# Kernel optimization log

Measured on AMD Instinct MI355X. Metric: run time of the kernel, lower is better.

The kernel has to match this reference:

```python
import jax, jax.numpy as jnp
import numpy as np

N, E, D, H, G, C = 50000, 600000, 128, 128, 512, 1000
HP = H // 5  # attention-MLP bottleneck (hidden_dim // 5)


def setup_inputs() -> dict:
    key = jax.random.key(0)
    ks = jax.random.split(key, 18)
    cfg_nodes = jax.random.normal(ks[0], (N, D), jnp.float32)
    cfg_relations = jax.random.randint(ks[1], (2, E), 0, N, dtype=jnp.int32)
    pos = jnp.sort(jax.random.randint(ks[2], (G + 1,), 0, N, dtype=jnp.int32))
    node_pos = pos.at[0].set(0).at[-1].set(N)

    def lin(k, fi, fo):
        return jax.random.normal(k, (fi, fo), jnp.float32) / np.sqrt(fi)

    return dict(
        cfg_nodes=cfg_nodes, cfg_relations=cfg_relations, node_pos=node_pos,
        # GATConv layer 1 (in=D, out=H, heads=1)
        W_g1=lin(ks[3], D, H),
        att_src1=jax.random.normal(ks[4], (H,), jnp.float32) / np.sqrt(H),
        att_dst1=jax.random.normal(ks[5], (H,), jnp.float32) / np.sqrt(H),
        b_g1=jnp.zeros((H,), jnp.float32),
        # GATConv layer 2 (in=H, out=H, heads=1, concat=False)
        W_g2=lin(ks[6], H, H),
        att_src2=jax.random.normal(ks[7], (H,), jnp.float32) / np.sqrt(H),
        att_dst2=jax.random.normal(ks[8], (H,), jnp.float32) / np.sqrt(H),
        b_g2=jnp.zeros((H,), jnp.float32),
        # GraphLocalAttention projection MLP
        Wp1=lin(ks[9], H, HP), bp1=jnp.zeros((HP,), jnp.float32),
        Wp2=jax.random.normal(ks[10], (HP,), jnp.float32) / np.sqrt(HP),
        bp2=jnp.zeros((), jnp.float32),
        # final classifier
        Wl=lin(ks[11], H, C), bl=jnp.zeros((C,), jnp.float32),
    )


def _gat_conv(x, src, dst, W, a_src, a_dst, b, n_nodes):
    # PyG GATConv (heads=1): h = xW; e_ij = LeakyReLU(a_s.h_j + a_d.h_i);
    # alpha = softmax over incoming edges of each target; out_i = sum alpha*h_j + b
    h = x @ W                                    # [N, F]
    as_ = h @ a_src                              # [N]
    ad_ = h @ a_dst                              # [N]
    e = jax.nn.leaky_relu(as_[src] + ad_[dst], 0.2)   # [E]
    m = jax.ops.segment_max(e, dst, num_segments=n_nodes)
    ex = jnp.exp(e - m[dst])
    s = jax.ops.segment_sum(ex, dst, num_segments=n_nodes)
    alpha = ex / s[dst]
    out = jax.ops.segment_sum(alpha[:, None] * h[src], dst, num_segments=n_nodes)
    return out + b


def reference(cfg_nodes, cfg_relations, node_pos,
              W_g1, att_src1, att_dst1, b_g1,
              W_g2, att_src2, att_dst2, b_g2,
              Wp1, bp1, Wp2, bp2, Wl, bl):
    n = cfg_nodes.shape[0]
    # add self-loops (PyG GATConv default)
    loops = jnp.arange(n, dtype=cfg_relations.dtype)
    src = jnp.concatenate([cfg_relations[0], loops])
    dst = jnp.concatenate([cfg_relations[1], loops])
    # dropout layers are identity in eval mode
    x = _gat_conv(cfg_nodes, src, dst, W_g1, att_src1, att_dst1, b_g1, n)
    x = jax.nn.elu(x)
    x = _gat_conv(x, src, dst, W_g2, att_src2, att_dst2, b_g2, n)
    # ragged segment attention pooling (attn_by_batch, fully vectorized)
    energy = jax.nn.relu(x @ Wp1 + bp1) @ Wp2 + bp2          # [N]
    seg = jnp.clip(jnp.searchsorted(node_pos, jnp.arange(n), side='right') - 1, 0, G - 1)
    m = jax.ops.segment_max(energy, seg, num_segments=G)
    ex = jnp.exp(energy - m[seg])
    s = jax.ops.segment_sum(ex, seg, num_segments=G)
    w = ex / s[seg]                                           # per-segment softmax
    pooled = jax.ops.segment_sum(w[:, None] * x, seg, num_segments=G)  # [G, H]
    return pooled @ Wl + bl                                   # [G, C]
```

## Files before the change

kernel.cpp:

```cpp
#include <hip/hip_runtime.h>
#include <hip/hip_bf16.h>
#include <math.h>

#define WAVE 64
#define GR 32

typedef __attribute__((ext_vector_type(8))) _Float16 half8;
typedef __attribute__((ext_vector_type(4))) float f32x4;
typedef __attribute__((ext_vector_type(4))) _Float16 half4;

__global__ void count_pack(const int* __restrict__ dst, int* __restrict__ deg, int E, int nbC,
                           const float* __restrict__ W1, const float* __restrict__ W2,
                           _Float16* __restrict__ W1h, _Float16* __restrict__ W2h,
                           const float* __restrict__ Wp1, int HP,
                           _Float16* __restrict__ Ph) {
    int b = blockIdx.x;
    if (b < nbC) {
        int e = (b * 256 + threadIdx.x) * 2;
        if (e + 1 < E) {
            int2 d = *(const int2*)(dst + e);
            atomicAdd(&deg[d.x], 1);
            atomicAdd(&deg[d.y], 1);
        } else if (e < E) {
            atomicAdd(&deg[dst[e]], 1);
        }
    } else if (b < nbC + 128) {
        int pb = b - nbC;
        const float* W = (pb >= 64) ? W2 : W1;
        _Float16* Hf = (pb >= 64) ? W2h : W1h;
        int idx = (pb & 63) * 256 + threadIdx.x;
        int j = idx & 7;
        int lane = (idx >> 3) & 63;
        int kc = (idx >> 9) & 3;
        int nt = idx >> 11;
        int k = kc * 32 + (lane >> 4) * 8 + j;
        int ncol = nt * 16 + (lane & 15);
        Hf[idx] = (_Float16)W[k * 128 + ncol];
    } else {
        int idx = (b - nbC - 128) * 256 + threadIdx.x;
        int j = idx & 7;
        int lane = (idx >> 3) & 63;
        int kc = (idx >> 9) & 3;
        int nt = idx >> 11;
        int k = kc * 32 + (lane >> 4) * 8 + j;
        int ncol = nt * 16 + (lane & 15);
        float x = (ncol < HP) ? Wp1[k * HP + ncol] : 0.f;
        Ph[idx] = (_Float16)x;
    }
}

__global__ void pack_wl(const float* __restrict__ Wl, int C, _Float16* __restrict__ Wlh) {
    int idx = blockIdx.x * 256 + threadIdx.x;
    int j = idx & 7;
    int lane = (idx >> 3) & 63;
    int kc = (idx >> 9) & 3;
    int nt = idx >> 11;
    int k = kc * 32 + (lane >> 4) * 8 + j;
    int ncol = nt * 16 + (lane & 15);
    float x = (ncol < C) ? Wl[(size_t)k * C + ncol] : 0.f;
    Wlh[idx] = (_Float16)x;
}

__global__ void scan_block(const int* __restrict__ in, int* __restrict__ part,
                           int* __restrict__ bsums, int n) {
    __shared__ int tmp[256];
    int tid = threadIdx.x;
    int i = blockIdx.x * 256 + tid;
    int v = (i < n) ? in[i] : 0;
    tmp[tid] = v;
    __syncthreads();
    for (int o = 1; o < 256; o <<= 1) {
        int t = (tid >= o) ? tmp[tid - o] : 0;
        __syncthreads();
        tmp[tid] += t;
        __syncthreads();
    }
    if (i < n) part[i] = tmp[tid] - v;
    if (tid == 255) bsums[blockIdx.x] = tmp[255];
}

__global__ void scan_finish(const int* __restrict__ part, const int* __restrict__ bsums,
                            int* __restrict__ offs, int* __restrict__ cursor,
                            int n, int Etot) {
    __shared__ int acc[256];
    int b = blockIdx.x, tid = threadIdx.x;
    int s = 0;
    for (int i = tid; i < b; i += 256) s += bsums[i];
    acc[tid] = s;
    __syncthreads();
    for (int o = 128; o > 0; o >>= 1) {
        if (tid < o) acc[tid] += acc[tid + o];
        __syncthreads();
    }
    int prefix = acc[0];
    int i = b * 256 + tid;
    if (i < n) {
        int v = part[i] + prefix;
        offs[i] = v;
        cursor[i] = v;
    }
    if (b == 0 && tid == 0) offs[n] = Etot;
}

__global__ void scatter_edges(const int* __restrict__ src, const int* __restrict__ dst,
                              int* __restrict__ cursor, int2* __restrict__ csr_sd, int E) {
    int e = (blockIdx.x * 256 + threadIdx.x) * 2;
    if (e + 1 < E) {
        int2 d = *(const int2*)(dst + e);
        int2 s = *(const int2*)(src + e);
        int p0 = atomicAdd(&cursor[d.x], 1);
        csr_sd[p0] = make_int2(s.x, d.x);
        int p1 = atomicAdd(&cursor[d.y], 1);
        csr_sd[p1] = make_int2(s.y, d.y);
    } else if (e < E) {
        int p = atomicAdd(&cursor[dst[e]], 1);
        csr_sd[p] = make_int2(src[e], dst[e]);
    }
}

__global__ __launch_bounds__(256) void gemm_mfma(const float* __restrict__ X,
                                                 const _Float16* __restrict__ Bh,
                                                 const float* __restrict__ a_s,
                                                 const float* __restrict__ a_d,
                                                 _Float16* __restrict__ Hout,
                                                 float* __restrict__ as_,
                                                 float* __restrict__ ad_, int n) {
    __shared__ char lds[GR * 136 * 4];
    _Float16* Xh = (_Float16*)lds;
    float* Hs = (float*)lds;

    int tid = threadIdx.x;
    int base = blockIdx.x * GR;
    const float4* X4 = (const float4*)X;

#pragma unroll
    for (int i = 0; i < 4; ++i) {
        int idx = i * 256 + tid;
        int row = idx >> 5, c4 = idx & 31;
        int rs = base + row; if (rs >= n) rs = n - 1;
        float4 v = X4[(size_t)rs * 32 + c4];
        half4 hv = {(_Float16)v.x, (_Float16)v.y, (_Float16)v.z, (_Float16)v.w};
        *(half4*)(Xh + row * 136 + c4 * 4) = hv;
    }
    __syncthreads();

    int wid = tid >> 6, lane = tid & 63;
    int quad = lane >> 4, l16 = lane & 15;
    int rowA = (wid & 1) * 16 + l16;
    int ntb = (wid >> 1) * 4;

    f32x4 acc[4];
#pragma unroll
    for (int t = 0; t < 4; ++t) acc[t] = (f32x4){0.f, 0.f, 0.f, 0.f};

    for (int kc = 0; kc < 4; ++kc) {
        half8 Ah = *(const half8*)(Xh + rowA * 136 + kc * 32 + quad * 8);
#pragma unroll
        for (int nt = 0; nt < 4; ++nt) {
            half8 Bv = *(const half8*)(Bh + (((size_t)((ntb + nt) * 4 + kc)) * 64 + lane) * 8);
            acc[nt] = __builtin_amdgcn_mfma_f32_16x16x32_f16(Ah, Bv, acc[nt], 0, 0, 0);
        }
    }
    __syncthreads();

    int rowD0 = (wid & 1) * 16 + quad * 4;
#pragma unroll
    for (int nt = 0; nt < 4; ++nt)
#pragma unroll
        for (int r = 0; r < 4; ++r)
            Hs[(rowD0 + r) * 136 + (ntb + nt) * 16 + l16] = acc[nt][r];
    __syncthreads();

    const float4* Hs4 = (const float4*)Hs;
    half4* H4 = (half4*)Hout;
#pragma unroll
    for (int i = 0; i < 4; ++i) {
        int idx = i * 256 + tid;
        int row = idx >> 5, c4 = idx & 31;
        int grow = base + row;
        if (grow < n) {
            float4 v = Hs4[row * 34 + c4];
            half4 hv = {(_Float16)v.x, (_Float16)v.y, (_Float16)v.z, (_Float16)v.w};
            H4[(size_t)grow * 32 + c4] = hv;
        }
    }

    int drow = tid >> 3, q = tid & 7;
    const float4* as4 = (const float4*)a_s;
    const float4* ad4 = (const float4*)a_d;
    float s = 0.f, d = 0.f;
#pragma unroll
    for (int j = 0; j < 4; ++j) {
        float4 v = Hs4[drow * 34 + q * 4 + j];
        float4 a = as4[q * 4 + j];
        float4 b = ad4[q * 4 + j];
        s += v.x * a.x + v.y * a.y + v.z * a.z + v.w * a.w;
        d += v.x * b.x + v.y * b.y + v.z * b.z + v.w * b.w;
    }
    s += __shfl_xor(s, 1, WAVE); s += __shfl_xor(s, 2, WAVE); s += __shfl_xor(s, 4, WAVE);
    d += __shfl_xor(d, 1, WAVE); d += __shfl_xor(d, 2, WAVE); d += __shfl_xor(d, 4, WAVE);
    if (q == 0 && base + drow < n) {
        as_[base + drow] = s;
        ad_[base + drow] = d;
    }
}

__global__ __launch_bounds__(256) void gemm_mfma_h(const _Float16* __restrict__ X,
                                                   const _Float16* __restrict__ Bh,
                                                   const float* __restrict__ a_s,
                                                   const float* __restrict__ a_d,
                                                   _Float16* __restrict__ Hout,
                                                   float* __restrict__ as_,
                                                   float* __restrict__ ad_, int n) {
    __shared__ char lds[GR * 136 * 4];
    _Float16* Xh = (_Float16*)lds;
    float* Hs = (float*)lds;

    int tid = threadIdx.x;
    int base = blockIdx.x * GR;
    const half8* X8 = (const half8*)X;

#pragma unroll
    for (int i = 0; i < 2; ++i) {
        int idx = i * 256 + tid;
        int row = idx >> 4, c8 = idx & 15;
        int rs = base + row; if (rs >= n) rs = n - 1;
        *(half8*)(Xh + row * 136 + c8 * 8) = X8[(size_t)rs * 16 + c8];
    }
    __syncthreads();

    int wid = tid >> 6, lane = tid & 63;
    int quad = lane >> 4, l16 = lane & 15;
    int rowA = (wid & 1) * 16 + l16;
    int ntb = (wid >> 1) * 4;

    f32x4 acc[4];
#pragma unroll
    for (int t = 0; t < 4; ++t) acc[t] = (f32x4){0.f, 0.f, 0.f, 0.f};

    for (int kc = 0; kc < 4; ++kc) {
        half8 Ah = *(const half8*)(Xh + rowA * 136 + kc * 32 + quad * 8);
#pragma unroll
        for (int nt = 0; nt < 4; ++nt) {
            half8 Bv = *(const half8*)(Bh + (((size_t)((ntb + nt) * 4 + kc)) * 64 + lane) * 8);
            acc[nt] = __builtin_amdgcn_mfma_f32_16x16x32_f16(Ah, Bv, acc[nt], 0, 0, 0);
        }
    }
    __syncthreads();

    int rowD0 = (wid & 1) * 16 + quad * 4;
#pragma unroll
    for (int nt = 0; nt < 4; ++nt)
#pragma unroll
        for (int r = 0; r < 4; ++r)
            Hs[(rowD0 + r) * 136 + (ntb + nt) * 16 + l16] = acc[nt][r];
    __syncthreads();

    const float4* Hs4 = (const float4*)Hs;
    half4* H4 = (half4*)Hout;
#pragma unroll
    for (int i = 0; i < 4; ++i) {
        int idx = i * 256 + tid;
        int row = idx >> 5, c4 = idx & 31;
        int grow = base + row;
        if (grow < n) {
            float4 v = Hs4[row * 34 + c4];
            half4 hv = {(_Float16)v.x, (_Float16)v.y, (_Float16)v.z, (_Float16)v.w};
            H4[(size_t)grow * 32 + c4] = hv;
        }
    }

    int drow = tid >> 3, q = tid & 7;
    const float4* as4 = (const float4*)a_s;
    const float4* ad4 = (const float4*)a_d;
    float s = 0.f, d = 0.f;
#pragma unroll
    for (int j = 0; j < 4; ++j) {
        float4 v = Hs4[drow * 34 + q * 4 + j];
        float4 a = as4[q * 4 + j];
        float4 b = ad4[q * 4 + j];
        s += v.x * a.x + v.y * a.y + v.z * a.z + v.w * a.w;
        d += v.x * b.x + v.y * b.y + v.z * b.z + v.w * b.w;
    }
    s += __shfl_xor(s, 1, WAVE); s += __shfl_xor(s, 2, WAVE); s += __shfl_xor(s, 4, WAVE);
    d += __shfl_xor(d, 1, WAVE); d += __shfl_xor(d, 2, WAVE); d += __shfl_xor(d, 4, WAVE);
    if (q == 0 && base + drow < n) {
        as_[base + drow] = s;
        ad_[base + drow] = d;
    }
}

__device__ __forceinline__ float leaky02(float x) { return x > 0.f ? x : 0.2f * x; }

__global__ __launch_bounds__(256) void edge_weights(const int2* __restrict__ csr_sd,
                                                    const float* __restrict__ as_,
                                                    const float* __restrict__ ad_,
                                                    int2* __restrict__ sw, int E) {
    int i = (blockIdx.x * 256 + threadIdx.x) * 4;
    if (i + 3 < E) {
        int4 p0 = *(const int4*)(csr_sd + i);
        int4 p1 = *(const int4*)(csr_sd + i + 2);
        float wx = __expf(leaky02(as_[p0.x] + ad_[p0.y]));
        float wy = __expf(leaky02(as_[p0.z] + ad_[p0.w]));
        float wz = __expf(leaky02(as_[p1.x] + ad_[p1.y]));
        float ww = __expf(leaky02(as_[p1.z] + ad_[p1.w]));
        int4 lo = make_int4(p0.x, __float_as_int(wx), p0.z, __float_as_int(wy));
        int4 hi = make_int4(p1.x, __float_as_int(wz), p1.z, __float_as_int(ww));
        *(int4*)(sw + i) = lo;
        *(int4*)(sw + i + 2) = hi;
    } else {
        for (; i < E; ++i) {
            int2 sd = csr_sd[i];
            float w = __expf(leaky02(as_[sd.x] + ad_[sd.y]));
            sw[i] = make_int2(sd.x, __float_as_int(w));
        }
    }
}

__global__ __launch_bounds__(256) void gat_aggregate(const _Float16* __restrict__ h,
                                                     const int2* __restrict__ sw,
                                                     const float* __restrict__ as_,
                                                     const float* __restrict__ ad_,
                                                     const int* __restrict__ offs,
                                                     const float* __restrict__ bias,
                                                     _Float16* __restrict__ out, int n, int act) {
    int node = blockIdx.x * 4 + (threadIdx.x >> 6);
    int lane = threadIdx.x & 63;
    if (node >= n) return;
    int beg = offs[node], end = offs[node + 1];
    int q4 = lane >> 4, l = lane & 15;
    const half8* h8 = (const half8*)h;

    float w_self = __expf(leaky02(as_[node] + ad_[node]));
    float facc[8], facc2[8];
    {
        half8 v = h8[(size_t)node * 16 + l];
        float ws = (q4 == 0) ? w_self : 0.f;
#pragma unroll
        for (int i = 0; i < 8; ++i) { facc[i] = ws * (float)v[i]; facc2[i] = 0.f; }
    }
    float sacc = (lane == 0) ? w_self : 0.f;
    for (int j = beg; j < end; j += 8) {
        int j0 = j + q4;
        int j1 = j + 4 + q4;
        bool vA = j0 < end;
        bool vB = j1 < end;
        int jA = vA ? j0 : (end - 1);
        int jB = vB ? j1 : (end - 1);
        int2 eA = sw[jA];
        int2 eB = sw[jB];
        int sA = vA ? eA.x : node;
        int sB = vB ? eB.x : node;
        float wA = vA ? __int_as_float(eA.y) : 0.f;
        float wB = vB ? __int_as_float(eB.y) : 0.f;
        half8 a = h8[(size_t)sA * 16 + l];
        half8 b = h8[(size_t)sB * 16 + l];
#pragma unroll
        for (int i = 0; i < 8; ++i) {
            facc[i]  = fmaf(wA, (float)a[i], facc[i]);
            facc2[i] = fmaf(wB, (float)b[i], facc2[i]);
        }
        sacc += (l == 0) ? (wA + wB) : 0.f;
    }
#pragma unroll
    for (int i = 0; i < 8; ++i) {
        facc[i] += facc2[i];
        facc[i] += __shfl_xor(facc[i], 16, WAVE);
        facc[i] += __shfl_xor(facc[i], 32, WAVE);
    }
    sacc += __shfl_xor(sacc, 16, WAVE);
    sacc += __shfl_xor(sacc, 32, WAVE);
    float inv_s = 1.f / __shfl(sacc, 0, WAVE);
    if (q4 == 0) {
        const float4* b4 = (const float4*)bias;
        float4 b0 = b4[l * 2], b1 = b4[l * 2 + 1];
        float o[8];
        o[0] = fmaf(facc[0], inv_s, b0.x);
        o[1] = fmaf(facc[1], inv_s, b0.y);
        o[2] = fmaf(facc[2], inv_s, b0.z);
        o[3] = fmaf(facc[3], inv_s, b0.w);
        o[4] = fmaf(facc[4], inv_s, b1.x);
        o[5] = fmaf(facc[5], inv_s, b1.y);
        o[6] = fmaf(facc[6], inv_s, b1.z);
        o[7] = fmaf(facc[7], inv_s, b1.w);
        if (act == 1) {
#pragma unroll
            for (int i = 0; i < 8; ++i) o[i] = o[i] > 0.f ? o[i] : expm1f(o[i]);
        }
        half8 hv;
#pragma unroll
        for (int i = 0; i < 8; ++i) hv[i] = (_Float16)o[i];
        ((half8*)(out + (size_t)node * 128))[l] = hv;
    }
}

#define GR2 64
__global__ __launch_bounds__(256) void energy_mfma(const _Float16* __restrict__ X,
                                                   const _Float16* __restrict__ Ph,
                                                   const float* __restrict__ bp1,
                                                   const float* __restrict__ Wp2,
                                                   const float* __restrict__ bp2,
                                                   float* __restrict__ energy, int n, int HP) {
    __shared__ _Float16 Xh[GR2 * 136];
    int tid = threadIdx.x;
    int base = blockIdx.x * GR2;
    const half8* X8 = (const half8*)X;
#pragma unroll
    for (int i = 0; i < 4; ++i) {
        int idx = i * 256 + tid;
        int row = idx >> 4, c8 = idx & 15;
        int rs = base + row; if (rs >= n) rs = n - 1;
        *(half8*)(Xh + row * 136 + c8 * 8) = X8[(size_t)rs * 16 + c8];
    }
    __syncthreads();

    int wid = tid >> 6, lane = tid & 63;
    int quad = lane >> 4, l16 = lane & 15;
    int rowA = wid * 16 + l16;

    f32x4 acc0 = (f32x4){0.f, 0.f, 0.f, 0.f};
    f32x4 acc1 = (f32x4){0.f, 0.f, 0.f, 0.f};
    for (int kc = 0; kc < 4; ++kc) {
        half8 Ah = *(const half8*)(Xh + rowA * 136 + kc * 32 + quad * 8);
        half8 B0 = *(const half8*)(Ph + (((size_t)kc) * 64 + lane) * 8);
        half8 B1 = *(const half8*)(Ph + (((size_t)(4 + kc)) * 64 + lane) * 8);
        acc0 = __builtin_amdgcn_mfma_f32_16x16x32_f16(Ah, B0, acc0, 0, 0, 0);
        acc1 = __builtin_amdgcn_mfma_f32_16x16x32_f16(Ah, B1, acc1, 0, 0, 0);
    }

    float b0 = bp1[l16];
    float w0 = Wp2[l16];
    int c1 = 16 + l16;
    int c1c = c1 < HP ? c1 : HP - 1;
    float b1 = bp1[c1c];
    float w1 = (c1 < HP) ? Wp2[c1c] : 0.f;
    float bp2v = bp2[0];
#pragma unroll
    for (int r = 0; r < 4; ++r) {
        float h0 = acc0[r] + b0;
        h0 = h0 > 0.f ? h0 : 0.f;
        float h1 = acc1[r] + b1;
        h1 = h1 > 0.f ? h1 : 0.f;
        float v = h0 * w0 + h1 * w1;
        v += __shfl_xor(v, 1, WAVE);
        v += __shfl_xor(v, 2, WAVE);
        v += __shfl_xor(v, 4, WAVE);
        v += __shfl_xor(v, 8, WAVE);
        int row = base + wid * 16 + quad * 4 + r;
        if (l16 == 0 && row < n) energy[row] = v + bp2v;
    }
}

__global__ __launch_bounds__(256) void seg_pool(const _Float16* __restrict__ X,
                                                const float* __restrict__ energy,
                                                const int* __restrict__ node_pos,
                                                float* __restrict__ pooled) {
    int g = blockIdx.x >> 1;
    int bn = blockIdx.x & 1;
    int beg = node_pos[g], end = node_pos[g + 1];
    int tid = threadIdx.x;
    int wid = tid >> 6, lane = tid & 63;
    __shared__ float swr[8];
    __shared__ float4 red[256];

    float m = -INFINITY;
    for (int i = beg + tid; i < end; i += 256) m = fmaxf(m, energy[i]);
#pragma unroll
    for (int o = 1; o < 64; o <<= 1) m = fmaxf(m, __shfl_xor(m, o, WAVE));
    if (lane == 0) swr[wid] = m;
    __syncthreads();
    m = fmaxf(fmaxf(swr[0], swr[1]), fmaxf(swr[2], swr[3]));

    float s = 0.f;
    for (int i = beg + tid; i < end; i += 256) s += __expf(energy[i] - m);
#pragma unroll
    for (int o = 1; o < 64; o <<= 1) s += __shfl_xor(s, o, WAVE);
    if (lane == 0) swr[4 + wid] = s;
    __syncthreads();
    s = swr[4] + swr[5] + swr[6] + swr[7];
    float inv = (end > beg && s > 0.f) ? 1.f / s : 0.f;

    int cq = tid & 15;
    int rg = tid >> 4;
    const half4* X4 = (const half4*)X;
    float4 acc = make_float4(0.f, 0.f, 0.f, 0.f);
#pragma unroll 2
    for (int i = beg + rg; i < end; i += 16) {
        float w = __expf(energy[i] - m) * inv;
        half4 v = X4[(size_t)i * 32 + bn * 16 + cq];
        acc.x = fmaf(w, (float)v.x, acc.x);
        acc.y = fmaf(w, (float)v.y, acc.y);
        acc.z = fmaf(w, (float)v.z, acc.z);
        acc.w = fmaf(w, (float)v.w, acc.w);
    }
    red[tid] = acc;
#pragma unroll
    for (int o = 8; o >= 1; o >>= 1) {
        __syncthreads();
        if (rg < o) {
            float4 t = red[tid + o * 16];
            acc.x += t.x; acc.y += t.y; acc.z += t.z; acc.w += t.w;
            red[tid] = acc;
        }
    }
    if (rg == 0)
        ((float4*)(pooled + (size_t)g * 128 + bn * 64))[cq] = acc;
}

__global__ __launch_bounds__(256) void classify_mfma(const float* __restrict__ P,
                                                     const _Float16* __restrict__ Wlh,
                                                     const float* __restrict__ bl,
                                                     float* __restrict__ out,
                                                     int G_, int C, int nbM) {
    __shared__ _Float16 Xh[GR * 136];
    int tid = threadIdx.x;
    int bm = blockIdx.x % nbM;
    int bn = blockIdx.x / nbM;
    int base = bm * GR;
    const float4* X4 = (const float4*)P;
#pragma unroll
    for (int i = 0; i < 4; ++i) {
        int idx = i * 256 + tid;
        int row = idx >> 5, c4 = idx & 31;
        int rs = base + row; if (rs >= G_) rs = G_ - 1;
        float4 v = X4[(size_t)rs * 32 + c4];
        half4 hv = {(_Float16)v.x, (_Float16)v.y, (_Float16)v.z, (_Float16)v.w};
        *(half4*)(Xh + row * 136 + c4 * 4) = hv;
    }
    __syncthreads();

    int wid = tid >> 6, lane = tid & 63;
    int quad = lane >> 4, l16 = lane & 15;
    int rowA = (wid & 1) * 16 + l16;
    int ntb = bn * 8 + (wid >> 1) * 4;

    f32x4 acc[4];
#pragma unroll
    for (int t = 0; t < 4; ++t) acc[t] = (f32x4){0.f, 0.f, 0.f, 0.f};

    for (int kc = 0; kc < 4; ++kc) {
        half8 Ah = *(const half8*)(Xh + rowA * 136 + kc * 32 + quad * 8);
#pragma unroll
        for (int nt = 0; nt < 4; ++nt) {
            half8 Bv = *(const half8*)(Wlh + (((size_t)((ntb + nt) * 4 + kc)) * 64 + lane) * 8);
            acc[nt] = __builtin_amdgcn_mfma_f32_16x16x32_f16(Ah, Bv, acc[nt], 0, 0, 0);
        }
    }

    int row0 = base + (wid & 1) * 16 + quad * 4;
#pragma unroll
    for (int nt = 0; nt < 4; ++nt) {
        int col = (ntb + nt) * 16 + l16;
        if (col < C) {
            float b = bl[col];
#pragma unroll
            for (int r = 0; r < 4; ++r) {
                int row = row0 + r;
                if (row < G_) out[(size_t)row * C + col] = acc[nt][r] + b;
            }
        }
    }
}

extern "C" void kernel_launch(void* const* d_in, const int* in_sizes, int n_in,
                              void* d_out, int out_size, void* d_ws, size_t ws_size,
                              hipStream_t stream) {
    const float* cfg_nodes = (const float*)d_in[0];
    const int* rel = (const int*)d_in[1];
    const int* node_pos = (const int*)d_in[2];
    const float* W_g1 = (const float*)d_in[3];
    const float* att_src1 = (const float*)d_in[4];
    const float* att_dst1 = (const float*)d_in[5];
    const float* b_g1 = (const float*)d_in[6];
    const float* W_g2 = (const float*)d_in[7];
    const float* att_src2 = (const float*)d_in[8];
    const float* att_dst2 = (const float*)d_in[9];
    const float* b_g2 = (const float*)d_in[10];
    const float* Wp1 = (const float*)d_in[11];
    const float* bp1 = (const float*)d_in[12];
    const float* Wp2 = (const float*)d_in[13];
    const float* bp2 = (const float*)d_in[14];
    const float* Wl = (const float*)d_in[15];
    const float* bl = (const float*)d_in[16];

    const int N = in_sizes[0] / 128;
    const int E = in_sizes[1] / 2;
    const int G = in_sizes[2] - 1;
    const int HP = in_sizes[12];
    const int C = out_size / G;

    const int* srcArr = rel;
    const int* dstArr = rel + E;

    char* w = (char*)d_ws;
    auto carve = [&](size_t bytes) -> char* {
        char* p = w;
        w += (bytes + 255) & ~(size_t)255;
        return p;
    };
    _Float16* bufH = (_Float16*)carve((size_t)N * 128 * 2);
    _Float16* bufF = (_Float16*)carve((size_t)N * 128 * 2);
    float* asv = (float*)carve((size_t)N * 4);
    float* adv = (float*)carve((size_t)N * 4);
    float* energy = (float*)carve((size_t)N * 4);
    int* deg = (int*)carve((size_t)N * 4);
    int* offs = (int*)carve((size_t)(N + 1) * 4);
    int* cursor = (int*)carve((size_t)N * 4);
    int2* csr_sd = (int2*)carve((size_t)E * 8);
    int2* swbuf = (int2*)carve((size_t)E * 8);
    int* bsums = (int*)carve(1024);
    _Float16* W1h = (_Float16*)carve(16384 * 2);
    _Float16* W2h = (_Float16*)carve(16384 * 2);
    _Float16* Ph = (_Float16*)carve(4096 * 2);
    _Float16* Wlh = (_Float16*)carve(131072 * 2);
    float* pooled = (float*)carve((size_t)G * 128 * 4);

    const int nbN = (N + 255) / 256;
    const int nbC = ((E + 1) / 2 + 255) / 256;
    const int nbT = (N + GR - 1) / GR;
    const int nbT2 = (N + GR2 - 1) / GR2;
    const int nbW = (E + 1023) / 1024;
    const int nbM = (G + GR - 1) / GR;
    const int nbCt = (C + 127) / 128;

    hipMemsetAsync(deg, 0, (size_t)N * 4, stream);
    count_pack<<<nbC + 144, 256, 0, stream>>>(dstArr, deg, E, nbC,
                                              W_g1, W_g2, W1h, W2h, Wp1, HP, Ph);
    pack_wl<<<512, 256, 0, stream>>>(Wl, C, Wlh);
    scan_block<<<nbN, 256, 0, stream>>>(deg, offs, bsums, N);
    scan_finish<<<nbN, 256, 0, stream>>>(offs, bsums, offs, cursor, N, E);
    scatter_edges<<<nbC, 256, 0, stream>>>(srcArr, dstArr, cursor, csr_sd, E);

    gemm_mfma<<<nbT, 256, 0, stream>>>(cfg_nodes, W1h, att_src1, att_dst1,
                                       bufH, asv, adv, N);
    edge_weights<<<nbW, 256, 0, stream>>>(csr_sd, asv, adv, swbuf, E);
    gat_aggregate<<<(N + 3) / 4, 256, 0, stream>>>(bufH, swbuf, asv, adv, offs, b_g1, bufF, N, 1);

    gemm_mfma_h<<<nbT, 256, 0, stream>>>(bufF, W2h, att_src2, att_dst2,
                                         bufH, asv, adv, N);
    edge_weights<<<nbW, 256, 0, stream>>>(csr_sd, asv, adv, swbuf, E);
    gat_aggregate<<<(N + 3) / 4, 256, 0, stream>>>(bufH, swbuf, asv, adv, offs, b_g2, bufF, N, 0);

    energy_mfma<<<nbT2, 256, 0, stream>>>(bufF, Ph, bp1, Wp2, bp2, energy, N, HP);
    seg_pool<<<G * 2, 256, 0, stream>>>(bufF, energy, node_pos, pooled);
    classify_mfma<<<nbM * nbCt, 256, 0, stream>>>(pooled, Wlh, bl, (float*)d_out, G, C, nbM);
}
```

Baseline: 298.6 us.

## Store CSR sources only and compute edge softmax weights inside aggregation

The CSR build now stores only source indices instead of (src,dst) pairs, and the scatter kernel processes eight edges per thread. edge_weights now only gathers as_[src] and packs it with the source, dropping the random ad_[dst] gather and the exp. The aggregation kernel adds the node's own ad_ value and applies leaky-ReLU and exp per edge. This cuts CSR memory traffic and one random gather per edge, at the cost of extra exp work in the aggregation inner loop.

```diff
diff --git a/kernel.cpp b/kernel.cpp
--- a/kernel.cpp
+++ b/kernel.cpp
@@ -103,18 +103,34 @@
 }
 
 __global__ void scatter_edges(const int* __restrict__ src, const int* __restrict__ dst,
-                              int* __restrict__ cursor, int2* __restrict__ csr_sd, int E) {
-    int e = (blockIdx.x * 256 + threadIdx.x) * 2;
-    if (e + 1 < E) {
-        int2 d = *(const int2*)(dst + e);
-        int2 s = *(const int2*)(src + e);
-        int p0 = atomicAdd(&cursor[d.x], 1);
-        csr_sd[p0] = make_int2(s.x, d.x);
-        int p1 = atomicAdd(&cursor[d.y], 1);
-        csr_sd[p1] = make_int2(s.y, d.y);
-    } else if (e < E) {
-        int p = atomicAdd(&cursor[dst[e]], 1);
-        csr_sd[p] = make_int2(src[e], dst[e]);
+                              int* __restrict__ cursor, int* __restrict__ csr_src, int E) {
+    int e0 = (blockIdx.x * 256 + threadIdx.x) * 8;
+    if (e0 + 7 < E) {
+        int4 d0 = *(const int4*)(dst + e0);
+        int4 d1 = *(const int4*)(dst + e0 + 4);
+        int4 s0 = *(const int4*)(src + e0);
+        int4 s1 = *(const int4*)(src + e0 + 4);
+        int p0 = atomicAdd(&cursor[d0.x], 1);
+        int p1 = atomicAdd(&cursor[d0.y], 1);
+        int p2 = atomicAdd(&cursor[d0.z], 1);
+        int p3 = atomicAdd(&cursor[d0.w], 1);
+        int p4 = atomicAdd(&cursor[d1.x], 1);
+        int p5 = atomicAdd(&cursor[d1.y], 1);
+        int p6 = atomicAdd(&cursor[d1.z], 1);
+        int p7 = atomicAdd(&cursor[d1.w], 1);
+        csr_src[p0] = s0.x;
+        csr_src[p1] = s0.y;
+        csr_src[p2] = s0.z;
+        csr_src[p3] = s0.w;
+        csr_src[p4] = s1.x;
+        csr_src[p5] = s1.y;
+        csr_src[p6] = s1.z;
+        csr_src[p7] = s1.w;
+    } else {
+        for (int e = e0; e < E; ++e) {
+            int p = atomicAdd(&cursor[dst[e]], 1);
+            csr_src[p] = src[e];
+        }
     }
 }
 
@@ -292,27 +308,24 @@
 
 __device__ __forceinline__ float leaky02(float x) { return x > 0.f ? x : 0.2f * x; }
 
-__global__ __launch_bounds__(256) void edge_weights(const int2* __restrict__ csr_sd,
+__global__ __launch_bounds__(256) void edge_weights(const int* __restrict__ csr_src,
                                                     const float* __restrict__ as_,
-                                                    const float* __restrict__ ad_,
                                                     int2* __restrict__ sw, int E) {
     int i = (blockIdx.x * 256 + threadIdx.x) * 4;
     if (i + 3 < E) {
-        int4 p0 = *(const int4*)(csr_sd + i);
-        int4 p1 = *(const int4*)(csr_sd + i + 2);
-        float wx = __expf(leaky02(as_[p0.x] + ad_[p0.y]));
-        float wy = __expf(leaky02(as_[p0.z] + ad_[p0.w]));
-        float wz = __expf(leaky02(as_[p1.x] + ad_[p1.y]));
-        float ww = __expf(leaky02(as_[p1.z] + ad_[p1.w]));
-        int4 lo = make_int4(p0.x, __float_as_int(wx), p0.z, __float_as_int(wy));
-        int4 hi = make_int4(p1.x, __float_as_int(wz), p1.z, __float_as_int(ww));
+        int4 s = *(const int4*)(csr_src + i);
+        float ax = as_[s.x];
+        float ay = as_[s.y];
+        float az = as_[s.z];
+        float aw = as_[s.w];
+        int4 lo = make_int4(s.x, __float_as_int(ax), s.y, __float_as_int(ay));
+        int4 hi = make_int4(s.z, __float_as_int(az), s.w, __float_as_int(aw));
         *(int4*)(sw + i) = lo;
         *(int4*)(sw + i + 2) = hi;
     } else {
         for (; i < E; ++i) {
-            int2 sd = csr_sd[i];
-            float w = __expf(leaky02(as_[sd.x] + ad_[sd.y]));
-            sw[i] = make_int2(sd.x, __float_as_int(w));
+            int s = csr_src[i];
+            sw[i] = make_int2(s, __float_as_int(as_[s]));
         }
     }
 }
@@ -331,7 +344,8 @@
     int q4 = lane >> 4, l = lane & 15;
     const half8* h8 = (const half8*)h;
 
-    float w_self = __expf(leaky02(as_[node] + ad_[node]));
+    float adn = ad_[node];
+    float w_self = __expf(leaky02(as_[node] + adn));
     float facc[8], facc2[8];
     {
         half8 v = h8[(size_t)node * 16 + l];
@@ -351,10 +365,10 @@
         int2 eB = sw[jB];
         int sA = vA ? eA.x : node;
         int sB = vB ? eB.x : node;
-        float wA = vA ? __int_as_float(eA.y) : 0.f;
-        float wB = vB ? __int_as_float(eB.y) : 0.f;
         half8 a = h8[(size_t)sA * 16 + l];
         half8 b = h8[(size_t)sB * 16 + l];
+        float wA = vA ? __expf(leaky02(__int_as_float(eA.y) + adn)) : 0.f;
+        float wB = vB ? __expf(leaky02(__int_as_float(eB.y) + adn)) : 0.f;
 #pragma unroll
         for (int i = 0; i < 8; ++i) {
             facc[i]  = fmaf(wA, (float)a[i], facc[i]);
@@ -606,7 +620,7 @@
     int* deg = (int*)carve((size_t)N * 4);
     int* offs = (int*)carve((size_t)(N + 1) * 4);
     int* cursor = (int*)carve((size_t)N * 4);
-    int2* csr_sd = (int2*)carve((size_t)E * 8);
+    int* csr_src = (int*)carve((size_t)E * 4);
     int2* swbuf = (int2*)carve((size_t)E * 8);
     int* bsums = (int*)carve(1024);
     _Float16* W1h = (_Float16*)carve(16384 * 2);
@@ -617,6 +631,7 @@
 
     const int nbN = (N + 255) / 256;
     const int nbC = ((E + 1) / 2 + 255) / 256;
+    const int nbS = ((E + 7) / 8 + 255) / 256;
     const int nbT = (N + GR - 1) / GR;
     const int nbT2 = (N + GR2 - 1) / GR2;
     const int nbW = (E + 1023) / 1024;
@@ -629,16 +644,16 @@
     pack_wl<<<512, 256, 0, stream>>>(Wl, C, Wlh);
     scan_block<<<nbN, 256, 0, stream>>>(deg, offs, bsums, N);
     scan_finish<<<nbN, 256, 0, stream>>>(offs, bsums, offs, cursor, N, E);
-    scatter_edges<<<nbC, 256, 0, stream>>>(srcArr, dstArr, cursor, csr_sd, E);
+    scatter_edges<<<nbS, 256, 0, stream>>>(srcArr, dstArr, cursor, csr_src, E);
 
     gemm_mfma<<<nbT, 256, 0, stream>>>(cfg_nodes, W1h, att_src1, att_dst1,
                                        bufH, asv, adv, N);
-    edge_weights<<<nbW, 256, 0, stream>>>(csr_sd, asv, adv, swbuf, E);
+    edge_weights<<<nbW, 256, 0, stream>>>(csr_src, asv, swbuf, E);
     gat_aggregate<<<(N + 3) / 4, 256, 0, stream>>>(bufH, swbuf, asv, adv, offs, b_g1, bufF, N, 1);
 
     gemm_mfma_h<<<nbT, 256, 0, stream>>>(bufF, W2h, att_src2, att_dst2,
                                          bufH, asv, adv, N);
-    edge_weights<<<nbW, 256, 0, stream>>>(csr_sd, asv, adv, swbuf, E);
+    edge_weights<<<nbW, 256, 0, stream>>>(csr_src, asv, swbuf, E);
     gat_aggregate<<<(N + 3) / 4, 256, 0, stream>>>(bufH, swbuf, asv, adv, offs, b_g2, bufF, N, 0);
 
     energy_mfma<<<nbT2, 256, 0, stream>>>(bufF, Ph, bp1, Wp2, bp2, energy, N, HP);
```

After: 295.0 us. About the same (-1.2%).
